# Kernel tuning notes

Hardware: AMD Instinct MI355X
Metric: run time of the kernel (lower is better)

Reference implementation:

```python
import jax, jax.numpy as jnp
import numpy as np

N, E, ELG, B = 50000, 400000, 1600000, 2000
F, ED, T = 64, 16, 6
SND = 6 * F  # LinearBlock hidden


def segment_softmax(x, seg, num_segments):
    m = jax.ops.segment_max(x, seg, num_segments=num_segments)
    e = jnp.exp(x - m[seg])
    s = jax.ops.segment_sum(e, seg, num_segments=num_segments)
    return e / (s[seg] + 1e-16)


def setup_inputs() -> dict:
    key = jax.random.key(0)
    ks = jax.random.split(key, 32)
    d = {}
    d['x'] = jax.random.normal(ks[0], (N, F), jnp.float32)
    d['edge_attr'] = jax.random.normal(ks[1], (E, ED), jnp.float32)
    d['edge_index'] = jax.random.randint(ks[2], (2, E), 0, N, jnp.int32)
    d['line_graph_edge_index'] = jax.random.randint(ks[3], (2, ELG), 0, E, jnp.int32)
    d['edge_index_batch'] = jnp.sort(jax.random.randint(ks[4], (E,), 0, B, jnp.int32))
    g = lambda k, shp, fi: jax.random.normal(k, shp, jnp.float32) * (1.0 / np.sqrt(fi))
    d['W_u'] = g(ks[5], (F, F), F)
    d['W_v'] = g(ks[6], (F, F), F)
    d['W_e'] = g(ks[7], (F, ED), ED)
    # GraphConv(F, 1): lin_rel (bias) on aggregated msgs + lin_root (no bias)
    d['conv_w_rel'] = g(ks[8], (1, F), F)
    d['conv_b_rel'] = jnp.zeros((1,), jnp.float32)
    d['conv_w_root'] = g(ks[9], (1, F), F)
    glorot_a = np.sqrt(6.0 / (F + T))
    d['a'] = jax.random.uniform(ks[10], (1, F, T), jnp.float32, -glorot_a, glorot_a)
    d['W_gout'] = g(ks[11], (F, F), F)
    d['b_gout'] = jnp.zeros((F,), jnp.float32)
    d['a_bias'] = jnp.zeros((1, 1, T), jnp.float32)
    d['lb1_w'] = g(ks[12], (SND, F), F); d['lb1_b'] = jnp.zeros((SND,), jnp.float32)
    d['lb2_w'] = g(ks[13], (SND, SND), SND); d['lb2_b'] = jnp.zeros((SND,), jnp.float32)
    d['lb3_w'] = g(ks[14], (SND, SND), SND); d['lb3_b'] = jnp.zeros((SND,), jnp.float32)
    d['lb4_w'] = g(ks[15], (SND, SND), SND); d['lb4_b'] = jnp.zeros((SND,), jnp.float32)
    d['lb5_w'] = g(ks[16], (F, SND), SND); d['lb5_b'] = jnp.zeros((F,), jnp.float32)
    return d


def reference(x, edge_attr, edge_index, line_graph_edge_index, edge_index_batch,
              W_u, W_v, W_e, conv_w_rel, conv_b_rel, conv_w_root,
              a, W_gout, b_gout, a_bias,
              lb1_w, lb1_b, lb2_w, lb2_b, lb3_w, lb3_b, lb4_w, lb4_b, lb5_w, lb5_b):
    src, dst = edge_index[0], edge_index[1]
    lsrc, ldst = line_graph_edge_index[0], line_graph_edge_index[1]
    # initial directed-edge features
    edge_feat = (x @ W_u.T)[src] + (x @ W_v.T)[dst] + edge_attr @ W_e.T  # [E,F]
    edge_feat = edge_feat / 3.0
    out = edge_feat
    outs, gouts = [], []
    for _ in range(T):  # fixed small iteration count
        agg = jax.ops.segment_sum(out[lsrc], ldst, num_segments=E)  # line-graph scatter-add
        out = edge_feat + agg
        # GlobalAttentionPool: GraphConv(F,1) on line graph, segment softmax, add-pool
        conv_agg = jax.ops.segment_sum(out[lsrc], ldst, num_segments=E)
        x_conv = conv_agg @ conv_w_rel.T + conv_b_rel + out @ conv_w_root.T  # [E,1]
        sc = segment_softmax(x_conv, edge_index_batch, B)  # [E,1]
        g = jax.ops.segment_sum(out * sc, edge_index_batch, num_segments=B)  # [B,F]
        outs.append(out)
        gouts.append(jnp.tanh(g @ W_gout.T + b_gout))
    gout_all = jnp.stack(gouts, axis=-1)  # [B,F,T]
    out_all = jnp.stack(outs, axis=-1)    # [E,F,T]
    scores = (gout_all * a).sum(1, keepdims=True) + a_bias  # [B,1,T]
    scores = jax.nn.softmax(scores, axis=-1)
    scores_e = scores[edge_index_batch]  # == repeat_interleave by degree (sorted batch)
    out_w = (out_all * scores_e).sum(-1)  # [E,F]
    h = x + jax.ops.segment_sum(out_w, dst, num_segments=N)
    # LinearBlock (SA-DDI lineage)
    h = jax.nn.relu(h @ lb1_w.T + lb1_b)
    h = (jax.nn.relu(h @ lb2_w.T + lb2_b) @ lb3_w.T + lb3_b + h) / 2.0
    h = (h @ lb4_w.T + lb4_b + h) / 2.0
    return jax.nn.relu(h @ lb5_w.T + lb5_b)
```

## Files before the change

### kernel.cpp

```cpp
#include <hip/hip_runtime.h>
#include <hip/hip_fp16.h>

#define N_   50000
#define E_   400000
#define ELG_ 1600000
#define B_   2000
#define F_   64
#define ED_  16
#define T_   6
#define SND_ 384

typedef long long ll;
typedef _Float16 f16x8 __attribute__((ext_vector_type(8)));
typedef float f32x4 __attribute__((ext_vector_type(4)));
typedef float fv4 __attribute__((ext_vector_type(4)));

__device__ inline float ldc(const float* p, ll i) { return p[i]; }
__device__ inline float ldc(const __half* p, ll i) { return __half2float(p[i]); }
__device__ inline void st1(float* p, float v) { *p = v; }
__device__ inline void st1(__half* p, float v) { *p = __float2half(v); }

template <int FPL>
__device__ inline void ldN(const float* p, float (&o)[FPL]) {
#pragma unroll
    for (int c = 0; c < FPL; c += 4) {
        fv4 v = *(const fv4*)(p + c);
        o[c] = v.x; o[c + 1] = v.y; o[c + 2] = v.z; o[c + 3] = v.w;
    }
}
template <int FPL>
__device__ inline void ldN(const __half* p, float (&o)[FPL]) {
#pragma unroll
    for (int c = 0; c < FPL; c += 8) {
        f16x8 raw = *(const f16x8*)(p + c);
#pragma unroll
        for (int i = 0; i < 8; i++) o[c + i] = (float)raw[i];
    }
}
template <int FPL>
__device__ inline void stN(float* p, const float (&v)[FPL]) {
#pragma unroll
    for (int c = 0; c < FPL; c += 4) {
        fv4 t; t.x = v[c]; t.y = v[c + 1]; t.z = v[c + 2]; t.w = v[c + 3];
        *(fv4*)(p + c) = t;
    }
}
template <int FPL>
__device__ inline void stN(__half* p, const float (&v)[FPL]) {
#pragma unroll
    for (int c = 0; c < FPL; c += 8) {
        f16x8 t;
#pragma unroll
        for (int i = 0; i < 8; i++) t[i] = (_Float16)v[c + i];
        *(f16x8*)(p + c) = t;
    }
}

__global__ __launch_bounds__(256) void k_count(const int* __restrict__ ldst, int* __restrict__ cnt) {
    int i = blockIdx.x * 256 + threadIdx.x;
    if (i < ELG_) atomicAdd(&cnt[ldst[i]], 1);
}

__global__ __launch_bounds__(256) void k_scan1(const int* __restrict__ cnt, int* __restrict__ rowptr,
                                               int* __restrict__ bsum) {
    __shared__ int s[256];
    int tid = threadIdx.x;
    int i = blockIdx.x * 256 + tid;
    int v = (i < E_) ? cnt[i] : 0;
    s[tid] = v;
    __syncthreads();
    for (int off = 1; off < 256; off <<= 1) {
        int t = (tid >= off) ? s[tid - off] : 0;
        __syncthreads();
        s[tid] += t;
        __syncthreads();
    }
    if (i < E_) rowptr[i] = s[tid] - v;
    if (tid == 255) bsum[blockIdx.x] = s[255];
}

__global__ __launch_bounds__(256) void k_scan2(int* __restrict__ bsum, int nb) {
    __shared__ int s[256];
    __shared__ int carry_s;
    int tid = threadIdx.x;
    if (tid == 0) carry_s = 0;
    __syncthreads();
    for (int base = 0; base < nb; base += 256) {
        int i = base + tid;
        int v = (i < nb) ? bsum[i] : 0;
        s[tid] = v;
        __syncthreads();
        for (int off = 1; off < 256; off <<= 1) {
            int t = (tid >= off) ? s[tid - off] : 0;
            __syncthreads();
            s[tid] += t;
            __syncthreads();
        }
        int c = carry_s;
        if (i < nb) bsum[i] = s[tid] - v + c;
        __syncthreads();
        if (tid == 0) carry_s = c + s[255];
        __syncthreads();
    }
}

__global__ __launch_bounds__(256) void k_scan3(int* __restrict__ rowptr, const int* __restrict__ bsum) {
    int i = blockIdx.x * 256 + threadIdx.x;
    if (i < E_) rowptr[i] += bsum[i >> 8];
    if (i == 0) rowptr[E_] = ELG_;
}

__global__ __launch_bounds__(256) void k_fill(const int* __restrict__ lsrc, const int* __restrict__ ldst,
                                              const int* __restrict__ rowptr, int* __restrict__ cursor,
                                              int* __restrict__ csr) {
    int i = blockIdx.x * 256 + threadIdx.x;
    if (i < ELG_) {
        int d = ldst[i];
        int pos = atomicAdd(&cursor[d], 1);
        csr[rowptr[d] + pos] = lsrc[i];
    }
}

__global__ __launch_bounds__(256) void k_bptr(const int* __restrict__ eib, int* __restrict__ bptr) {
    int b = blockIdx.x * 256 + threadIdx.x;
    if (b > B_) return;
    int lo = 0, hi = E_;
    while (lo < hi) {
        int mid = (lo + hi) >> 1;
        if (eib[mid] < b) lo = mid + 1; else hi = mid;
    }
    bptr[b] = lo;
}

__global__ __launch_bounds__(256) void k_xuv(const float* __restrict__ x,
                                             const float* __restrict__ Wu, const float* __restrict__ Wv,
                                             float* __restrict__ xu, float* __restrict__ xv) {
    __shared__ float wus[64 * 65];
    __shared__ float wvs[64 * 65];
    __shared__ float xs[16][64];
    int tid = threadIdx.x;
    for (int i = tid; i < 4096; i += 256) {
        int f = i >> 6, k = i & 63;
        wus[k * 65 + f] = Wu[i];
        wvs[k * 65 + f] = Wv[i];
    }
    int r0 = blockIdx.x * 16;
    for (int i = tid; i < 16 * 64; i += 256) {
        int r = i >> 6, j = i & 63;
        int row = r0 + r;
        xs[r][j] = (row < N_) ? x[(ll)row * 64 + j] : 0.f;
    }
    __syncthreads();
    int j = tid & 63, lr0 = tid >> 6;
    float su[4] = {0, 0, 0, 0}, sv[4] = {0, 0, 0, 0};
    for (int k = 0; k < 64; k++) {
        float wu = wus[k * 65 + j];
        float wv = wvs[k * 65 + j];
#pragma unroll
        for (int r = 0; r < 4; r++) {
            float xr = xs[lr0 + r * 4][k];
            su[r] += xr * wu;
            sv[r] += xr * wv;
        }
    }
#pragma unroll
    for (int r = 0; r < 4; r++) {
        int row = r0 + lr0 + r * 4;
        if (row < N_) {
            xu[(ll)row * 64 + j] = su[r];
            xv[(ll)row * 64 + j] = sv[r];
        }
    }
}

template <typename ET>
__global__ __launch_bounds__(256) void k_ef(const float* __restrict__ xu, const float* __restrict__ xv,
                                            const float* __restrict__ ea, const float* __restrict__ We,
                                            const int* __restrict__ src, const int* __restrict__ dst,
                                            ET* __restrict__ ef) {
    __shared__ float wes[16 * 65];
    int tid = threadIdx.x;
    for (int i = tid; i < 1024; i += 256) {
        wes[(i & 15) * 65 + (i >> 4)] = We[i];
    }
    __syncthreads();
    int wid = tid >> 6, f = tid & 63;
    ll e0 = (ll)blockIdx.x * 16;
#pragma unroll
    for (int r = 0; r < 4; r++) {
        ll e = e0 + wid + r * 4;
        if (e >= E_) return;
        int s = src[e], d = dst[e];
        float v = xu[(ll)s * 64 + f] + xv[(ll)d * 64 + f];
#pragma unroll
        for (int k = 0; k < 16; k++) v += ea[e * 16 + k] * wes[k * 65 + f];
        st1(&ef[e * 64 + f], v * (1.0f / 3.0f));
    }
}

template <typename T, typename OT, bool WOUT, bool WXC, int ACC>
__global__ __launch_bounds__(256) void k_segv(
    const T* __restrict__ state, T* __restrict__ nxt, OT* __restrict__ outw,
    const float* __restrict__ xu, const float* __restrict__ xv,
    const float* __restrict__ ea, const float* __restrict__ We,
    const int* __restrict__ esrc, const int* __restrict__ edst,
    const int* __restrict__ rowptr, const int* __restrict__ csr,
    float* __restrict__ xc, const float* __restrict__ w_rel,
    const float* __restrict__ b_rel, const float* __restrict__ w_root,
    const float* __restrict__ scores, const int* __restrict__ eib, int tslot)
{
    constexpr int FPL = 16 / sizeof(T);
    constexpr int LPR = F_ / FPL;
    constexpr int RPB = 256 / LPR;
    constexpr bool EF = WOUT || (ACC > 0);
    __shared__ float wes[16 * 65];
    int tid = threadIdx.x;
    if (EF) {
        for (int i = tid; i < 1024; i += 256)
            wes[(i & 15) * 65 + (i >> 4)] = We[i];
        __syncthreads();
    }
    int sub = tid % LPR;
    int r   = tid / LPR;
    ll d = (ll)blockIdx.x * RPB + r;
    int f0 = sub * FPL;
    int p0 = rowptr[d], p1 = rowptr[d + 1];
    float acc[FPL], acc2[FPL];
#pragma unroll
    for (int j = 0; j < FPL; j++) { acc[j] = 0.f; acc2[j] = 0.f; }
    int p = p0;
    for (; p + 4 <= p1; p += 4) {
        int s0 = csr[p], s1 = csr[p + 1], s2 = csr[p + 2], s3 = csr[p + 3];
        float v0[FPL], v1[FPL], v2[FPL], v3[FPL];
        ldN<FPL>(&state[(ll)s0 * F_ + f0], v0);
        ldN<FPL>(&state[(ll)s1 * F_ + f0], v1);
        ldN<FPL>(&state[(ll)s2 * F_ + f0], v2);
        ldN<FPL>(&state[(ll)s3 * F_ + f0], v3);
#pragma unroll
        for (int j = 0; j < FPL; j++) { acc[j] += v0[j] + v2[j]; acc2[j] += v1[j] + v3[j]; }
    }
    for (; p + 2 <= p1; p += 2) {
        int s0 = csr[p], s1 = csr[p + 1];
        float v0[FPL], v1[FPL];
        ldN<FPL>(&state[(ll)s0 * F_ + f0], v0);
        ldN<FPL>(&state[(ll)s1 * F_ + f0], v1);
#pragma unroll
        for (int j = 0; j < FPL; j++) { acc[j] += v0[j]; acc2[j] += v1[j]; }
    }
    if (p < p1) {
        int s0 = csr[p];
        float v0[FPL];
        ldN<FPL>(&state[(ll)s0 * F_ + f0], v0);
#pragma unroll
        for (int j = 0; j < FPL; j++) acc[j] += v0[j];
    }
#pragma unroll
    for (int j = 0; j < FPL; j++) acc[j] += acc2[j];
    if (EF) {
        int se = esrc[d], de = edst[d];
        float o[FPL], xuv[FPL], xvv[FPL];
        ldN<FPL>(&xu[(ll)se * 64 + f0], xuv);
        ldN<FPL>(&xv[(ll)de * 64 + f0], xvv);
#pragma unroll
        for (int j = 0; j < FPL; j++) o[j] = xuv[j] + xvv[j];
#pragma unroll
        for (int k = 0; k < 16; k++) {
            float eav = ea[d * 16 + k];
#pragma unroll
            for (int j = 0; j < FPL; j++) o[j] += eav * wes[k * 65 + f0 + j];
        }
#pragma unroll
        for (int j = 0; j < FPL; j++) o[j] = o[j] * (1.0f / 3.0f) + acc[j];
        if (WOUT) stN<FPL>(&nxt[(ll)d * F_ + f0], o);
        if (ACC > 0) {
            float w = scores[eib[d] * 6 + tslot];
            float ow[FPL];
            if (ACC == 2) ldN<FPL>(&outw[(ll)d * F_ + f0], ow);
            else {
#pragma unroll
                for (int j = 0; j < FPL; j++) ow[j] = 0.f;
            }
#pragma unroll
            for (int j = 0; j < FPL; j++) ow[j] += w * o[j];
            stN<FPL>(&outw[(ll)d * F_ + f0], ow);
        }
    }
    if (WXC) {
        float ov[FPL];
        ldN<FPL>(&state[(ll)d * F_ + f0], ov);
        float part = 0.f;
#pragma unroll
        for (int j = 0; j < FPL; j++)
            part += acc[j] * w_rel[f0 + j] + ov[j] * w_root[f0 + j];
#pragma unroll
        for (int off = LPR / 2; off; off >>= 1) part += __shfl_xor(part, off, 64);
        if (sub == 0) xc[d] = part + b_rel[0];
    }
}

template <typename TA, typename TB, typename OT>
__global__ __launch_bounds__(256) void k_comb(const TA* __restrict__ o6, const TB* __restrict__ o5,
                                              OT* __restrict__ outw, const float* __restrict__ scores,
                                              const int* __restrict__ eib) {
    ll i = (ll)blockIdx.x * 256 + threadIdx.x;
    if (i >= (ll)E_ * 64) return;
    int e = (int)(i >> 6);
    int b = eib[e];
    float v = scores[b * 6 + 4] * ldc(o5, i) + scores[b * 6 + 5] * ldc(o6, i);
    st1(&outw[i], v);
}

template <typename ST>
__global__ __launch_bounds__(256) void k_pool(const float* __restrict__ xc, const ST* __restrict__ out_t,
                                              const int* __restrict__ bptr, const float* __restrict__ Wg,
                                              const float* __restrict__ bg, float* __restrict__ gouts,
                                              int tslot) {
    int b = blockIdx.x;
    int tid = threadIdx.x;
    int p0 = bptr[b], p1 = bptr[b + 1];
    __shared__ float red[256];
    __shared__ float gsh[64];
    float m = -1e30f;
    for (int i = p0 + tid; i < p1; i += 256) m = fmaxf(m, xc[i]);
    red[tid] = m;
    __syncthreads();
    for (int o = 128; o; o >>= 1) { if (tid < o) red[tid] = fmaxf(red[tid], red[tid + o]); __syncthreads(); }
    m = red[0];
    __syncthreads();
    float ss = 0.f;
    for (int i = p0 + tid; i < p1; i += 256) ss += __expf(xc[i] - m);
    red[tid] = ss;
    __syncthreads();
    for (int o = 128; o; o >>= 1) { if (tid < o) red[tid] += red[tid + o]; __syncthreads(); }
    float inv = 1.0f / (red[0] + 1e-16f);
    __syncthreads();
    int lane = tid & 63, grp = tid >> 6;
    float acc = 0.f;
    for (int e = p0 + grp; e < p1; e += 4) {
        float w = __expf(xc[e] - m) * inv;
        acc += ldc(out_t, (ll)e * 64 + lane) * w;
    }
    red[tid] = acc;
    __syncthreads();
    if (tid < 64) gsh[tid] = red[tid] + red[tid + 64] + red[tid + 128] + red[tid + 192];
    __syncthreads();
    if (tid < 64) {
        float z = bg[tid];
#pragma unroll 8
        for (int k = 0; k < 64; k++) z += gsh[k] * Wg[tid * 64 + k];
        gouts[((ll)b * T_ + tslot) * 64 + tid] = tanhf(z);
    }
}

__global__ __launch_bounds__(64) void k_scores(const float* __restrict__ gouts, const float* __restrict__ a,
                                               const float* __restrict__ ab, float* __restrict__ scores) {
    int b = blockIdx.x, f = threadIdx.x;
    float lg[6];
#pragma unroll
    for (int t = 0; t < 6; t++) {
        float v = gouts[((ll)b * T_ + t) * 64 + f] * a[f * 6 + t];
#pragma unroll
        for (int o = 32; o; o >>= 1) v += __shfl_xor(v, o, 64);
        lg[t] = v + ab[t];
    }
    float m = lg[0];
#pragma unroll
    for (int t = 1; t < 6; t++) m = fmaxf(m, lg[t]);
    float s = 0.f;
#pragma unroll
    for (int t = 0; t < 6; t++) { lg[t] = __expf(lg[t] - m); s += lg[t]; }
    if (f == 0) {
        float inv = 1.0f / s;
#pragma unroll
        for (int t = 0; t < 6; t++) scores[b * 6 + t] = lg[t] * inv;
    }
}

__global__ __launch_bounds__(256) void k_copy(const float* __restrict__ in, float* __restrict__ out, int n) {
    int i = blockIdx.x * 256 + threadIdx.x;
    if (i < n) out[i] = in[i];
}

__global__ __launch_bounds__(256) void k_zero(float* __restrict__ out, int n) {
    int i = blockIdx.x * 256 + threadIdx.x;
    if (i < n) out[i] = 0.f;
}

__global__ __launch_bounds__(256) void k_f2h(const float* __restrict__ in, __half* __restrict__ out, int n) {
    int i = blockIdx.x * 256 + threadIdx.x;
    if (i < n) out[i] = __float2half(in[i]);
}

template <typename OT>
__global__ __launch_bounds__(256) void k_scatter(const OT* __restrict__ outw, const int* __restrict__ dst,
                                                 float* __restrict__ h) {
    ll i = (ll)blockIdx.x * 256 + threadIdx.x;
    if (i >= (ll)E_ * 64) return;
    int e = (int)(i >> 6), f = (int)(i & 63);
    atomicAdd(&h[(ll)dst[e] * 64 + f], ldc(outw, i));
}

template <int MODE, typename CT>
__global__ __launch_bounds__(256) void k_gemm_h(
    const __half* __restrict__ Ah, const __half* __restrict__ Wh,
    const float* __restrict__ bias, const __half* __restrict__ R,
    CT* __restrict__ C, int M, int K, int Nc)
{
    __shared__ _Float16 As[64][40];
    __shared__ _Float16 Ws[64][40];
    int tid = threadIdx.x;
    int m0 = blockIdx.x * 64, j0 = blockIdx.y * 64;
    int wv = tid >> 6, lane = tid & 63;
    int srow = tid >> 2, skq = tid & 3;
    f32x4 acc[4] = {};
    const int arow = m0 + srow;
    for (int k0 = 0; k0 < K; k0 += 32) {
        f16x8 a8 = {};
        if (arow < M) a8 = *(const f16x8*)&Ah[(ll)arow * K + k0 + skq * 8];
        *(f16x8*)&As[srow][skq * 8] = a8;
        f16x8 w8 = *(const f16x8*)&Wh[(ll)(j0 + srow) * K + k0 + skq * 8];
        *(f16x8*)&Ws[srow][skq * 8] = w8;
        __syncthreads();
        f16x8 af = *(const f16x8*)&As[wv * 16 + (lane & 15)][(lane >> 4) * 8];
#pragma unroll
        for (int nt = 0; nt < 4; nt++) {
            f16x8 bf = *(const f16x8*)&Ws[nt * 16 + (lane & 15)][(lane >> 4) * 8];
            acc[nt] = __builtin_amdgcn_mfma_f32_16x16x32_f16(af, bf, acc[nt], 0, 0, 0);
        }
        __syncthreads();
    }
    int colb = lane & 15;
    int row0 = m0 + wv * 16 + (lane >> 4) * 4;
#pragma unroll
    for (int nt = 0; nt < 4; nt++) {
        int col = j0 + nt * 16 + colb;
#pragma unroll
        for (int rg = 0; rg < 4; rg++) {
            int row = row0 + rg;
            if (row >= M) continue;
            float z = acc[nt][rg] + bias[col];
            float o;
            if (MODE == 0) o = fmaxf(z, 0.f);
            else o = (z + __half2float(R[(ll)row * Nc + col])) * 0.5f;
            st1(&C[(ll)row * Nc + col], o);
        }
    }
}

template <int MODE>
__global__ __launch_bounds__(256) void k_gemm(const float* __restrict__ A, const float* __restrict__ W,
                                              const float* __restrict__ bias, const float* __restrict__ R,
                                              float* __restrict__ C, int M, int K, int Nc) {
    __shared__ float As[64][68];
    __shared__ float Ws[64][68];
    int tid = threadIdx.x;
    int m0 = blockIdx.x * 64, j0 = blockIdx.y * 64;
    int tx = tid & 15, ty = tid >> 4;
    float acc[4][4];
#pragma unroll
    for (int i = 0; i < 4; i++)
#pragma unroll
        for (int j = 0; j < 4; j++) acc[i][j] = 0.f;
    for (int k0 = 0; k0 < K; k0 += 64) {
#pragma unroll
        for (int l = 0; l < 4; l++) {
            int fi = tid + l * 256;
            int m = fi >> 4, kq = fi & 15;
            int row = m0 + m;
            float4 v = make_float4(0.f, 0.f, 0.f, 0.f);
            if (row < M) v = *(const float4*)&A[(ll)row * K + k0 + kq * 4];
            As[kq * 4 + 0][m] = v.x; As[kq * 4 + 1][m] = v.y;
            As[kq * 4 + 2][m] = v.z; As[kq * 4 + 3][m] = v.w;
            float4 w = *(const float4*)&W[(ll)(j0 + m) * K + k0 + kq * 4];
            Ws[kq * 4 + 0][m] = w.x; Ws[kq * 4 + 1][m] = w.y;
            Ws[kq * 4 + 2][m] = w.z; Ws[kq * 4 + 3][m] = w.w;
        }
        __syncthreads();
#pragma unroll
        for (int k = 0; k < 64; k++) {
            float4 av = *(const float4*)&As[k][ty * 4];
            float4 bv = *(const float4*)&Ws[k][tx * 4];
            float a_[4] = {av.x, av.y, av.z, av.w};
            float b_[4] = {bv.x, bv.y, bv.z, bv.w};
#pragma unroll
            for (int i = 0; i < 4; i++)
#pragma unroll
                for (int j = 0; j < 4; j++) acc[i][j] += a_[i] * b_[j];
        }
        __syncthreads();
    }
#pragma unroll
    for (int i = 0; i < 4; i++) {
        int row = m0 + ty * 4 + i;
        if (row >= M) continue;
#pragma unroll
        for (int j = 0; j < 4; j++) {
            int col = j0 + tx * 4 + j;
            float z = acc[i][j] + bias[col];
            float o;
            if (MODE == 0) o = fmaxf(z, 0.f);
            else o = (z + R[(ll)row * Nc + col]) * 0.5f;
            C[(ll)row * Nc + col] = o;
        }
    }
}

struct Args {
    const float *x, *ea;
    const int *src, *dstp, *lsrc, *ldst, *eib;
    const float *Wu, *Wv, *We, *w_rel, *b_rel, *w_root, *a, *Wg, *bg, *abias;
    const float *lb1w, *lb1b, *lb2w, *lb2b, *lb3w, *lb3b, *lb4w, *lb4b, *lb5w, *lb5b;
    float *xc, *gouts, *scores;
    int *rowptr, *cnt, *csr, *bsum, *bptr;
    float *xu, *xv;
    float *h;
    char *ws_base;
};

template <typename T1T, typename OT>
static void run_tier(const Args& A, T1T* bufA, T1T* bufB, __half* q0, __half* q1, OT* outw,
                     bool bigLB, hipStream_t stream) {
    constexpr int RPB1 = 256 / (F_ / (16 / (int)sizeof(T1T)));
    const int sg1 = E_ / RPB1;
    const int sg2 = E_ / 32;
    const int efg = (E_ + 15) / 16;
    const int ewg = (int)(((ll)E_ * 64 + 255) / 256);

    k_xuv<<<(N_ + 15) / 16, 256, 0, stream>>>(A.x, A.Wu, A.Wv, A.xu, A.xv);
    k_ef<T1T><<<efg, 256, 0, stream>>>(A.xu, A.xv, A.ea, A.We, A.src, A.dstp, bufA);

#define SEGARGS A.xu, A.xv, A.ea, A.We, A.src, A.dstp, A.rowptr, A.csr, \
                A.xc, A.w_rel, A.b_rel, A.w_root, A.scores, A.eib
    k_segv<T1T, OT, true,  false, 0><<<sg1, 256, 0, stream>>>(bufA, bufB, (OT*)nullptr, SEGARGS, 0);
    k_segv<T1T, OT, true,  true,  0><<<sg1, 256, 0, stream>>>(bufB, bufA, (OT*)nullptr, SEGARGS, 0);
    k_pool<T1T><<<B_, 256, 0, stream>>>(A.xc, bufB, A.bptr, A.Wg, A.bg, A.gouts, 0);
    k_segv<T1T, OT, true,  true,  0><<<sg1, 256, 0, stream>>>(bufA, bufB, (OT*)nullptr, SEGARGS, 0);
    k_pool<T1T><<<B_, 256, 0, stream>>>(A.xc, bufA, A.bptr, A.Wg, A.bg, A.gouts, 1);
    k_segv<T1T, OT, true,  true,  0><<<sg1, 256, 0, stream>>>(bufB, bufA, (OT*)nullptr, SEGARGS, 0);
    k_pool<T1T><<<B_, 256, 0, stream>>>(A.xc, bufB, A.bptr, A.Wg, A.bg, A.gouts, 2);
    k_segv<T1T, OT, true,  true,  0><<<sg1, 256, 0, stream>>>(bufA, bufB, (OT*)nullptr, SEGARGS, 0);
    k_pool<T1T><<<B_, 256, 0, stream>>>(A.xc, bufA, A.bptr, A.Wg, A.bg, A.gouts, 3);
    k_segv<T1T, OT, true,  true,  0><<<sg1, 256, 0, stream>>>(bufB, bufA, (OT*)nullptr, SEGARGS, 0);
    k_pool<T1T><<<B_, 256, 0, stream>>>(A.xc, bufB, A.bptr, A.Wg, A.bg, A.gouts, 4);
    k_segv<T1T, OT, false, true,  0><<<sg1, 256, 0, stream>>>(bufA, (T1T*)nullptr, (OT*)nullptr, SEGARGS, 0);
    k_pool<T1T><<<B_, 256, 0, stream>>>(A.xc, bufA, A.bptr, A.Wg, A.bg, A.gouts, 5);

    k_scores<<<B_, 64, 0, stream>>>(A.gouts, A.a, A.abias, A.scores);

    k_comb<T1T, T1T, OT><<<ewg, 256, 0, stream>>>(bufA, bufB, outw, A.scores, A.eib);
    k_ef<__half><<<efg, 256, 0, stream>>>(A.xu, A.xv, A.ea, A.We, A.src, A.dstp, q0);
    k_segv<__half, OT, true,  false, 2><<<sg2, 256, 0, stream>>>(q0, q1, outw, SEGARGS, 0);
    k_segv<__half, OT, true,  false, 2><<<sg2, 256, 0, stream>>>(q1, q0, outw, SEGARGS, 1);
    k_segv<__half, OT, true,  false, 2><<<sg2, 256, 0, stream>>>(q0, q1, outw, SEGARGS, 2);
    k_segv<__half, OT, false, false, 2><<<sg2, 256, 0, stream>>>(q1, (__half*)nullptr, outw, SEGARGS, 3);
#undef SEGARGS

    k_copy<<<(N_ * 64 + 255) / 256, 256, 0, stream>>>(A.x, A.h, N_ * 64);
    k_scatter<OT><<<ewg, 256, 0, stream>>>(outw, A.dstp, A.h);

    if (bigLB) {
        __half* hf  = (__half*)A.ws_base;
        __half* w1h = hf  + (size_t)N_ * 64;
        __half* w2h = w1h + (size_t)SND_ * 64;
        __half* w3h = w2h + (size_t)SND_ * SND_;
        __half* w4h = w3h + (size_t)SND_ * SND_;
        __half* w5h = w4h + (size_t)SND_ * SND_;
        __half* hb1 = w5h + (size_t)64 * SND_;
        __half* hb2 = hb1 + (size_t)N_ * SND_;
        __half* hb3 = hb2 + (size_t)N_ * SND_;
        __half* hb4 = hb3 + (size_t)N_ * SND_;
        k_f2h<<<(N_ * 64 + 255) / 256, 256, 0, stream>>>(A.h, hf, N_ * 64);
        k_f2h<<<(SND_ * 64 + 255) / 256, 256, 0, stream>>>(A.lb1w, w1h, SND_ * 64);
        k_f2h<<<(SND_ * SND_ + 255) / 256, 256, 0, stream>>>(A.lb2w, w2h, SND_ * SND_);
        k_f2h<<<(SND_ * SND_ + 255) / 256, 256, 0, stream>>>(A.lb3w, w3h, SND_ * SND_);
        k_f2h<<<(SND_ * SND_ + 255) / 256, 256, 0, stream>>>(A.lb4w, w4h, SND_ * SND_);
        k_f2h<<<(SND_ * 64 + 255) / 256, 256, 0, stream>>>(A.lb5w, w5h, 64 * SND_);
        dim3 g6((N_ + 63) / 64, SND_ / 64);
        dim3 g1((N_ + 63) / 64, 1);
        k_gemm_h<0, __half><<<g6, 256, 0, stream>>>(hf,  w1h, A.lb1b, nullptr, hb1, N_, 64,   SND_);
        k_gemm_h<0, __half><<<g6, 256, 0, stream>>>(hb1, w2h, A.lb2b, nullptr, hb2, N_, SND_, SND_);
        k_gemm_h<1, __half><<<g6, 256, 0, stream>>>(hb2, w3h, A.lb3b, hb1,    hb3, N_, SND_, SND_);
        k_gemm_h<1, __half><<<g6, 256, 0, stream>>>(hb3, w4h, A.lb4b, hb3,    hb4, N_, SND_, SND_);
        k_gemm_h<0, float ><<<g1, 256, 0, stream>>>(hb4, w5h, A.lb5b, nullptr, A.h, N_, SND_, 64);
    } else {
        const int CH = 12800;
        size_t cb = (size_t)CH * SND_ * 4;
        float* b1 = (float*)A.ws_base;
        float* b2 = (float*)(A.ws_base + cb);
        float* b3 = (float*)(A.ws_base + 2 * cb);
        for (int r0 = 0; r0 < N_; r0 += CH) {
            int m = (N_ - r0 < CH) ? (N_ - r0) : CH;
            dim3 g6((m + 63) / 64, SND_ / 64);
            dim3 g1((m + 63) / 64, 1);
            k_gemm<0><<<g6, 256, 0, stream>>>(A.h + (ll)r0 * 64, A.lb1w, A.lb1b, nullptr, b1, m, 64,   SND_);
            k_gemm<0><<<g6, 256, 0, stream>>>(b1, A.lb2w, A.lb2b, nullptr, b2, m, SND_, SND_);
            k_gemm<1><<<g6, 256, 0, stream>>>(b2, A.lb3w, A.lb3b, b1,      b3, m, SND_, SND_);
            k_gemm<1><<<g6, 256, 0, stream>>>(b3, A.lb4w, A.lb4b, b3,      b1, m, SND_, SND_);
            k_gemm<0><<<g1, 256, 0, stream>>>(b1, A.lb5w, A.lb5b, nullptr, A.h + (ll)r0 * 64, m, SND_, 64);
        }
    }
}

extern "C" void kernel_launch(void* const* d_in, const int* in_sizes, int n_in,
                              void* d_out, int out_size, void* d_ws, size_t ws_size,
                              hipStream_t stream) {
    (void)in_sizes; (void)n_in; (void)out_size;
    Args A;
    A.x      = (const float*)d_in[0];
    A.ea     = (const float*)d_in[1];
    const int* eidx = (const int*)d_in[2];
    const int* lgp  = (const int*)d_in[3];
    A.eib    = (const int*)d_in[4];
    A.Wu     = (const float*)d_in[5];
    A.Wv     = (const float*)d_in[6];
    A.We     = (const float*)d_in[7];
    A.w_rel  = (const float*)d_in[8];
    A.b_rel  = (const float*)d_in[9];
    A.w_root = (const float*)d_in[10];
    A.a      = (const float*)d_in[11];
    A.Wg     = (const float*)d_in[12];
    A.bg     = (const float*)d_in[13];
    A.abias  = (const float*)d_in[14];
    A.lb1w = (const float*)d_in[15]; A.lb1b = (const float*)d_in[16];
    A.lb2w = (const float*)d_in[17]; A.lb2b = (const float*)d_in[18];
    A.lb3w = (const float*)d_in[19]; A.lb3b = (const float*)d_in[20];
    A.lb4w = (const float*)d_in[21]; A.lb4b = (const float*)d_in[22];
    A.lb5w = (const float*)d_in[23]; A.lb5b = (const float*)d_in[24];
    A.src  = eidx;
    A.dstp = eidx + E_;
    A.lsrc = lgp;
    A.ldst = lgp + ELG_;
    A.h       = (float*)d_out;
    A.ws_base = (char*)d_ws;

    char* p = (char*)d_ws;
    auto alloc = [&](size_t bytes) -> char* {
        char* r = p;
        p += (bytes + 255) & ~(size_t)255;
        return r;
    };
    A.xc     = (float*)alloc((size_t)E_ * 4);
    A.gouts  = (float*)alloc((size_t)B_ * T_ * 64 * 4);
    A.scores = (float*)alloc((size_t)B_ * T_ * 4);
    A.rowptr = (int*)alloc((size_t)(E_ + 1) * 4);
    A.cnt    = (int*)alloc((size_t)E_ * 4);
    A.csr    = (int*)alloc((size_t)ELG_ * 4);
    A.bsum   = (int*)alloc(8192);
    A.bptr   = (int*)alloc((size_t)(B_ + 1) * 4);
    A.xu     = (float*)alloc((size_t)N_ * 64 * 4);
    A.xv     = (float*)alloc((size_t)N_ * 64 * 4);

    const size_t NEED_T1 = 244736768ull;
    const size_t NEED_T3 = 193536768ull;

    if (ws_size < NEED_T3) {
        k_zero<<<(N_ * 64 + 255) / 256, 256, 0, stream>>>((float*)d_out, N_ * 64);
        return;
    }

    hipMemsetAsync(A.cnt, 0, (size_t)E_ * 4, stream);
    k_count<<<(ELG_ + 255) / 256, 256, 0, stream>>>(A.ldst, A.cnt);
    int nb1 = (E_ + 255) / 256;
    k_scan1<<<nb1, 256, 0, stream>>>(A.cnt, A.rowptr, A.bsum);
    k_scan2<<<1, 256, 0, stream>>>(A.bsum, nb1);
    k_scan3<<<nb1, 256, 0, stream>>>(A.rowptr, A.bsum);
    hipMemsetAsync(A.cnt, 0, (size_t)E_ * 4, stream);
    k_fill<<<(ELG_ + 255) / 256, 256, 0, stream>>>(A.lsrc, A.ldst, A.rowptr, A.cnt, A.csr);
    k_bptr<<<(B_ + 1 + 255) / 256, 256, 0, stream>>>(A.eib, A.bptr);

    if (ws_size >= NEED_T1) {
        float* bufA = (float*)alloc((size_t)E_ * 64 * 4);
        float* bufB = (float*)alloc((size_t)E_ * 64 * 4);
        __half* q0 = (__half*)bufA;
        __half* q1 = q0 + (size_t)E_ * 64;
        run_tier<float, float>(A, bufA, bufB, q0, q1, (float*)bufB, true, stream);
    } else {
        __half* bufA = (__half*)alloc((size_t)E_ * 64 * 2);
        __half* bufB = (__half*)alloc((size_t)E_ * 64 * 2);
        __half* outw = (__half*)alloc((size_t)E_ * 64 * 2);
        run_tier<__half, __half>(A, bufA, bufB, bufA, bufB, outw, false, stream);
    }
}
```

Measured before the change: 2.096 ms.

## Compute full 384-wide output rows per block in fp16 LinearBlock GEMMs

Each GEMM block in the fp16 LinearBlock path now computes the whole output width (24 MFMA fragments = 384 columns) for its 64 rows, instead of tiling columns over a second grid dimension. The A tile is loaded once per row block, not once per column tile, which removes the redundant activation reads. In exchange each block holds 24 accumulator fragments and a larger shared W tile. That raises register and LDS pressure, lowers occupancy, and shrinks the grid to about 782 blocks.

Result: slower. 2.225 ms (+6.2%).

```diff
diff --git a/kernel.cpp b/kernel.cpp
--- a/kernel.cpp
+++ b/kernel.cpp
@@ -400,30 +400,34 @@
     atomicAdd(&h[(ll)dst[e] * 64 + f], ldc(outw, i));
 }
 
-template <int MODE, typename CT>
-__global__ __launch_bounds__(256) void k_gemm_h(
+template <int NFRAG, int MODE, typename CT>
+__global__ __launch_bounds__(256) void k_gemm_w(
     const __half* __restrict__ Ah, const __half* __restrict__ Wh,
     const float* __restrict__ bias, const __half* __restrict__ R,
-    CT* __restrict__ C, int M, int K, int Nc)
+    CT* __restrict__ C, int M, int K)
 {
+    constexpr int NC = NFRAG * 16;
     __shared__ _Float16 As[64][40];
-    __shared__ _Float16 Ws[64][40];
-    int tid = threadIdx.x;
-    int m0 = blockIdx.x * 64, j0 = blockIdx.y * 64;
+    __shared__ _Float16 Ws[NC][40];
+    int tid = threadIdx.x;
+    int m0 = blockIdx.x * 64;
     int wv = tid >> 6, lane = tid & 63;
     int srow = tid >> 2, skq = tid & 3;
-    f32x4 acc[4] = {};
+    f32x4 acc[NFRAG] = {};
     const int arow = m0 + srow;
     for (int k0 = 0; k0 < K; k0 += 32) {
         f16x8 a8 = {};
         if (arow < M) a8 = *(const f16x8*)&Ah[(ll)arow * K + k0 + skq * 8];
         *(f16x8*)&As[srow][skq * 8] = a8;
-        f16x8 w8 = *(const f16x8*)&Wh[(ll)(j0 + srow) * K + k0 + skq * 8];
-        *(f16x8*)&Ws[srow][skq * 8] = w8;
+        for (int i = tid; i < NC * 4; i += 256) {
+            int wrow = i >> 2, wkq = i & 3;
+            f16x8 w8 = *(const f16x8*)&Wh[(ll)wrow * K + k0 + wkq * 8];
+            *(f16x8*)&Ws[wrow][wkq * 8] = w8;
+        }
         __syncthreads();
         f16x8 af = *(const f16x8*)&As[wv * 16 + (lane & 15)][(lane >> 4) * 8];
 #pragma unroll
-        for (int nt = 0; nt < 4; nt++) {
+        for (int nt = 0; nt < NFRAG; nt++) {
             f16x8 bf = *(const f16x8*)&Ws[nt * 16 + (lane & 15)][(lane >> 4) * 8];
             acc[nt] = __builtin_amdgcn_mfma_f32_16x16x32_f16(af, bf, acc[nt], 0, 0, 0);
         }
@@ -432,8 +436,8 @@
     int colb = lane & 15;
     int row0 = m0 + wv * 16 + (lane >> 4) * 4;
 #pragma unroll
-    for (int nt = 0; nt < 4; nt++) {
-        int col = j0 + nt * 16 + colb;
+    for (int nt = 0; nt < NFRAG; nt++) {
+        int col = nt * 16 + colb;
 #pragma unroll
         for (int rg = 0; rg < 4; rg++) {
             int row = row0 + rg;
@@ -441,8 +445,8 @@
             float z = acc[nt][rg] + bias[col];
             float o;
             if (MODE == 0) o = fmaxf(z, 0.f);
-            else o = (z + __half2float(R[(ll)row * Nc + col])) * 0.5f;
-            st1(&C[(ll)row * Nc + col], o);
+            else o = (z + __half2float(R[(ll)row * NC + col])) * 0.5f;
+            st1(&C[(ll)row * NC + col], o);
         }
     }
 }
@@ -575,13 +579,12 @@
         k_f2h<<<(SND_ * SND_ + 255) / 256, 256, 0, stream>>>(A.lb3w, w3h, SND_ * SND_);
         k_f2h<<<(SND_ * SND_ + 255) / 256, 256, 0, stream>>>(A.lb4w, w4h, SND_ * SND_);
         k_f2h<<<(SND_ * 64 + 255) / 256, 256, 0, stream>>>(A.lb5w, w5h, 64 * SND_);
-        dim3 g6((N_ + 63) / 64, SND_ / 64);
-        dim3 g1((N_ + 63) / 64, 1);
-        k_gemm_h<0, __half><<<g6, 256, 0, stream>>>(hf,  w1h, A.lb1b, nullptr, hb1, N_, 64,   SND_);
-        k_gemm_h<0, __half><<<g6, 256, 0, stream>>>(hb1, w2h, A.lb2b, nullptr, hb2, N_, SND_, SND_);
-        k_gemm_h<1, __half><<<g6, 256, 0, stream>>>(hb2, w3h, A.lb3b, hb1,    hb3, N_, SND_, SND_);
-        k_gemm_h<1, __half><<<g6, 256, 0, stream>>>(hb3, w4h, A.lb4b, hb3,    hb4, N_, SND_, SND_);
-        k_gemm_h<0, float ><<<g1, 256, 0, stream>>>(hb4, w5h, A.lb5b, nullptr, A.h, N_, SND_, 64);
+        int gb = (N_ + 63) / 64;
+        k_gemm_w<24, 0, __half><<<gb, 256, 0, stream>>>(hf,  w1h, A.lb1b, nullptr, hb1, N_, 64);
+        k_gemm_w<24, 0, __half><<<gb, 256, 0, stream>>>(hb1, w2h, A.lb2b, nullptr, hb2, N_, SND_);
+        k_gemm_w<24, 1, __half><<<gb, 256, 0, stream>>>(hb2, w3h, A.lb3b, hb1,    hb3, N_, SND_);
+        k_gemm_w<24, 1, __half><<<gb, 256, 0, stream>>>(hb3, w4h, A.lb4b, hb3,    hb4, N_, SND_);
+        k_gemm_w<4,  0, float ><<<gb, 256, 0, stream>>>(hb4, w5h, A.lb5b, nullptr, A.h, N_, SND_);
     } else {
         const int CH = 12800;
         size_t cb = (size_t)CH * SND_ * 4;
```

## Scatter weighted tier outputs directly into h, dropping the intermediate outw buffer

Applied to the files above, without the earlier changes.

In the large-workspace path, the last four tiers now keep their fp16 outputs in four separate buffers instead of accumulating into outw inside each segv pass. The score-weighted sum is then done in two fused scatter kernels: one for tiers 5-6 right after scoring, one for tiers 1-4 at the end. Both atomically add into h, which replaces the separate combine and scatter passes and the read-modify-write of outw in every segv. The cost is twice as many atomic scatters over E*64 elements and more live fp16 buffers. Reusing bufB as q2/q3 after k_scat2 has consumed it depends on stream ordering.

Measured after the change: 2.029 ms. -3.2%, faster.

```diff
diff --git a/kernel.cpp b/kernel.cpp
--- a/kernel.cpp
+++ b/kernel.cpp
@@ -310,6 +310,30 @@
     st1(&outw[i], v);
 }
 
+template <typename TA>
+__global__ __launch_bounds__(256) void k_scat2(const TA* __restrict__ o6, const TA* __restrict__ o5,
+                                               const float* __restrict__ scores, const int* __restrict__ eib,
+                                               const int* __restrict__ dst, float* __restrict__ h) {
+    ll i = (ll)blockIdx.x * 256 + threadIdx.x;
+    if (i >= (ll)E_ * 64) return;
+    int e = (int)(i >> 6), f = (int)(i & 63);
+    int b = eib[e];
+    float v = scores[b * 6 + 4] * ldc(o5, i) + scores[b * 6 + 5] * ldc(o6, i);
+    atomicAdd(&h[(ll)dst[e] * 64 + f], v);
+}
+
+__global__ __launch_bounds__(256) void k_scat4(const __half* __restrict__ o1, const __half* __restrict__ o2,
+                                               const __half* __restrict__ o3, const __half* __restrict__ o4,
+                                               const float* __restrict__ scores, const int* __restrict__ eib,
+                                               const int* __restrict__ dst, float* __restrict__ h) {
+    ll i = (ll)blockIdx.x * 256 + threadIdx.x;
+    if (i >= (ll)E_ * 64) return;
+    int e = (int)(i >> 6), f = (int)(i & 63);
+    const float* sc = &scores[eib[e] * 6];
+    float v = sc[0] * ldc(o1, i) + sc[1] * ldc(o2, i) + sc[2] * ldc(o3, i) + sc[3] * ldc(o4, i);
+    atomicAdd(&h[(ll)dst[e] * 64 + f], v);
+}
+
 template <typename ST>
 __global__ __launch_bounds__(256) void k_pool(const float* __restrict__ xc, const ST* __restrict__ out_t,
                                               const int* __restrict__ bptr, const float* __restrict__ Wg,
@@ -518,8 +542,9 @@
 };
 
 template <typename T1T, typename OT>
-static void run_tier(const Args& A, T1T* bufA, T1T* bufB, __half* q0, __half* q1, OT* outw,
-                     bool bigLB, hipStream_t stream) {
+static void run_tier(const Args& A, T1T* bufA, T1T* bufB,
+                     __half* q0, __half* q1, __half* q2, __half* q3,
+                     OT* outw, bool bigLB, hipStream_t stream) {
     constexpr int RPB1 = 256 / (F_ / (16 / (int)sizeof(T1T)));
     const int sg1 = E_ / RPB1;
     const int sg2 = E_ / 32;
@@ -547,16 +572,26 @@
 
     k_scores<<<B_, 64, 0, stream>>>(A.gouts, A.a, A.abias, A.scores);
 
-    k_comb<T1T, T1T, OT><<<ewg, 256, 0, stream>>>(bufA, bufB, outw, A.scores, A.eib);
-    k_ef<__half><<<efg, 256, 0, stream>>>(A.xu, A.xv, A.ea, A.We, A.src, A.dstp, q0);
-    k_segv<__half, OT, true,  false, 2><<<sg2, 256, 0, stream>>>(q0, q1, outw, SEGARGS, 0);
-    k_segv<__half, OT, true,  false, 2><<<sg2, 256, 0, stream>>>(q1, q0, outw, SEGARGS, 1);
-    k_segv<__half, OT, true,  false, 2><<<sg2, 256, 0, stream>>>(q0, q1, outw, SEGARGS, 2);
-    k_segv<__half, OT, false, false, 2><<<sg2, 256, 0, stream>>>(q1, (__half*)nullptr, outw, SEGARGS, 3);
+    k_copy<<<(N_ * 64 + 255) / 256, 256, 0, stream>>>(A.x, A.h, N_ * 64);
+
+    if (q2) {
+        k_scat2<T1T><<<ewg, 256, 0, stream>>>(bufA, bufB, A.scores, A.eib, A.dstp, A.h);
+        k_ef<__half><<<efg, 256, 0, stream>>>(A.xu, A.xv, A.ea, A.We, A.src, A.dstp, q0);
+        k_segv<__half, OT, true, false, 0><<<sg2, 256, 0, stream>>>(q0, q1, (OT*)nullptr, SEGARGS, 0);
+        k_segv<__half, OT, true, false, 0><<<sg2, 256, 0, stream>>>(q1, q2, (OT*)nullptr, SEGARGS, 0);
+        k_segv<__half, OT, true, false, 0><<<sg2, 256, 0, stream>>>(q2, q3, (OT*)nullptr, SEGARGS, 0);
+        k_segv<__half, OT, true, false, 0><<<sg2, 256, 0, stream>>>(q3, q0, (OT*)nullptr, SEGARGS, 0);
+        k_scat4<<<ewg, 256, 0, stream>>>(q1, q2, q3, q0, A.scores, A.eib, A.dstp, A.h);
+    } else {
+        k_comb<T1T, T1T, OT><<<ewg, 256, 0, stream>>>(bufA, bufB, outw, A.scores, A.eib);
+        k_ef<__half><<<efg, 256, 0, stream>>>(A.xu, A.xv, A.ea, A.We, A.src, A.dstp, q0);
+        k_segv<__half, OT, true,  false, 2><<<sg2, 256, 0, stream>>>(q0, q1, outw, SEGARGS, 0);
+        k_segv<__half, OT, true,  false, 2><<<sg2, 256, 0, stream>>>(q1, q0, outw, SEGARGS, 1);
+        k_segv<__half, OT, true,  false, 2><<<sg2, 256, 0, stream>>>(q0, q1, outw, SEGARGS, 2);
+        k_segv<__half, OT, false, false, 2><<<sg2, 256, 0, stream>>>(q1, (__half*)nullptr, outw, SEGARGS, 3);
+        k_scatter<OT><<<ewg, 256, 0, stream>>>(outw, A.dstp, A.h);
+    }
 #undef SEGARGS
-
-    k_copy<<<(N_ * 64 + 255) / 256, 256, 0, stream>>>(A.x, A.h, N_ * 64);
-    k_scatter<OT><<<ewg, 256, 0, stream>>>(outw, A.dstp, A.h);
 
     if (bigLB) {
         __half* hf  = (__half*)A.ws_base;
@@ -673,11 +708,14 @@
         float* bufB = (float*)alloc((size_t)E_ * 64 * 4);
         __half* q0 = (__half*)bufA;
         __half* q1 = q0 + (size_t)E_ * 64;
-        run_tier<float, float>(A, bufA, bufB, q0, q1, (float*)bufB, true, stream);
+        __half* q2 = (__half*)bufB;
+        __half* q3 = q2 + (size_t)E_ * 64;
+        run_tier<float, float>(A, bufA, bufB, q0, q1, q2, q3, (float*)nullptr, true, stream);
     } else {
         __half* bufA = (__half*)alloc((size_t)E_ * 64 * 2);
         __half* bufB = (__half*)alloc((size_t)E_ * 64 * 2);
         __half* outw = (__half*)alloc((size_t)E_ * 64 * 2);
-        run_tier<__half, __half>(A, bufA, bufB, bufA, bufB, outw, false, stream);
-    }
-}
+        run_tier<__half, __half>(A, bufA, bufB, bufA, bufB, (__half*)nullptr, (__half*)nullptr,
+                                 outw, false, stream);
+    }
+}
```
